# Optimization experiments

Hardware: AMD Instinct MI355X
Metric: run time of the kernel (lower is better)

The kernel has to match this reference:

```python
import jax, jax.numpy as jnp
import numpy as np
from functools import partial

# dims matching init_kwargs
H = 512      # hidden_size
F = 2048     # ff_size
NH = 8       # num_heads
NL = 6       # num_layers
V = 1024     # vocab_size
T = 8        # sentence_length
S = 5        # n_sentences_in_paragraph
P = 16       # n_paragraphs_in_article
L = P * S * T          # article_length = 640
N = L + 1              # sequence length used by masks = 641
B = 16                 # batch
HD = H // NH           # head dim
LN_EPS = 1e-5
NEG = -1e9


def _build_mask():
    # pseudo_causal_masks[0] from the torch __init__: causal ~tril plus
    # blocking of within-paragraph sentence-0 key columns.
    a = np.ones((P, S, T, P, S, T), dtype=bool)
    j = np.arange(P)
    a[j, :, :, j, 0, :] = False
    a = a.reshape(L, L)
    causal = ~np.tril(np.ones((N, N), dtype=bool))
    m = causal.copy()
    m[:-1, 1:] = np.logical_and(a, causal[:-1, 1:])
    return m  # True = disallowed


def _build_pe():
    # sinusoidal pe exactly as in __init__ (div_term uses hidden_size in denom)
    pos = np.arange(N, dtype=np.float32)[:, None]
    div = np.exp(np.arange(0, H // 2, dtype=np.float32) * (-np.log(10000.0) / H))
    pe = np.zeros((N, H), dtype=np.float32)
    pe[:, 0::2] = np.sin(pos * div)
    pe[:, 1::2] = np.cos(pos * div)
    return pe


def setup_inputs() -> dict:
    key = jax.random.key(0)
    ks = jax.random.split(key, 12)
    sd = 0.02
    inp = {
        'tokens': jax.random.randint(ks[0], (B, N), 0, V),
        'attn_mask': jnp.asarray(_build_mask()),
        'pe': jnp.asarray(_build_pe()),
        'emb': jax.random.normal(ks[1], (V, H), jnp.float32) * sd,
        'qkv_w': jax.random.normal(ks[2], (NL, 3 * H, H), jnp.float32) * sd,
        'qkv_b': jnp.zeros((NL, 3 * H), jnp.float32),
        'out_w': jax.random.normal(ks[3], (NL, H, H), jnp.float32) * sd,
        'out_b': jnp.zeros((NL, H), jnp.float32),
        'ln1_g': jnp.ones((NL, H), jnp.float32),
        'ln1_b': jnp.zeros((NL, H), jnp.float32),
        'fc1_w': jax.random.normal(ks[4], (NL, F, H), jnp.float32) * sd,
        'fc1_b': jnp.zeros((NL, F), jnp.float32),
        'fc2_w': jax.random.normal(ks[5], (NL, H, F), jnp.float32) * sd,
        'fc2_b': jnp.zeros((NL, H), jnp.float32),
        'ln2_g': jnp.ones((NL, H), jnp.float32),
        'ln2_b': jnp.zeros((NL, H), jnp.float32),
        'lnf_g': jnp.ones((H,), jnp.float32),
        'lnf_b': jnp.zeros((H,), jnp.float32),
        'dep_w': jax.random.normal(ks[6], (V, H), jnp.float32) * sd,
        'dep_b': jnp.zeros((V,), jnp.float32),
    }
    return inp


def _ln(x, g, b):
    m = jnp.mean(x, axis=-1, keepdims=True)
    v = jnp.mean(jnp.square(x - m), axis=-1, keepdims=True)
    return (x - m) * jax.lax.rsqrt(v + LN_EPS) * g + b


def _encoder_layer(x, p, mask):
    qw, qb, ow, ob, g1, b1, w1, bb1, w2, bb2, g2, b2 = p
    Bsz, Nn, _ = x.shape
    qkv = x @ qw.T + qb                                   # [B,N,3H]
    q, k, v = jnp.split(qkv, 3, axis=-1)
    q = q.reshape(Bsz, Nn, NH, HD)
    k = k.reshape(Bsz, Nn, NH, HD)
    v = v.reshape(Bsz, Nn, NH, HD)
    scores = jnp.einsum('bqhd,bkhd->bhqk', q, k) / jnp.sqrt(jnp.asarray(HD, x.dtype))
    scores = jnp.where(mask[None, None], NEG, scores)
    att = jax.nn.softmax(scores, axis=-1)
    o = jnp.einsum('bhqk,bkhd->bqhd', att, v).reshape(Bsz, Nn, H)
    o = o @ ow.T + ob
    x = _ln(x + o, g1, b1)                                # post-LN (torch default)
    f = jax.nn.gelu(x @ w1.T + bb1, approximate=False) @ w2.T + bb2
    return _ln(x + f, g2, b2)


def reference(tokens, attn_mask, pe, emb, qkv_w, qkv_b, out_w, out_b,
              ln1_g, ln1_b, fc1_w, fc1_b, fc2_w, fc2_b, ln2_g, ln2_b,
              lnf_g, lnf_b, dep_w, dep_b):
    x = emb[tokens] + pe[None]                            # [B,N,H]
    layers = (qkv_w, qkv_b, out_w, out_b, ln1_g, ln1_b,
              fc1_w, fc1_b, fc2_w, fc2_b, ln2_g, ln2_b)

    def step(h, p):
        return _encoder_layer(h, p, attn_mask), None

    x, _ = jax.lax.scan(step, x, layers)
    x = _ln(x, lnf_g, lnf_b)
    return x @ dep_w.T + dep_b                            # [B,N,V] logits
```

## Files before the change

kernel.cpp:

```cpp
#include <hip/hip_runtime.h>
#include <stdint.h>

#define NSEQ 641
#define BATCH 16
#define MROWS (BATCH * NSEQ)
#define HID 512
#define FFD 2048
#define NHEAD 8
#define HDIM 64
#define NLAYER 6
#define VOCAB 1024
#define KPAD 704

typedef __bf16 bf16x8 __attribute__((ext_vector_type(8)));
typedef float  f32x4  __attribute__((ext_vector_type(4)));
typedef int    i32x4  __attribute__((ext_vector_type(4)));
typedef short  s16x8  __attribute__((ext_vector_type(8)));
typedef short  s16x4  __attribute__((ext_vector_type(4)));

#define EXP_C 0.18033688011112042f

__device__ __forceinline__ uint32_t swz(uint32_t b) { return b ^ (((b >> 7) & 7u) << 4); }

__device__ __forceinline__ unsigned short f2bf(float f) {
  uint32_t u = __builtin_bit_cast(uint32_t, f);
  u += 0x7FFFu + ((u >> 16) & 1u);
  return (unsigned short)(u >> 16);
}

__device__ __forceinline__ void gload16(const void* g, void* l) {
  __builtin_amdgcn_global_load_lds(
      (const __attribute__((address_space(1))) uint32_t*)g,
      (__attribute__((address_space(3))) uint32_t*)l, 16, 0, 0);
}

__device__ __forceinline__ bf16x8 ld_lds16(const void* p) {
  return __builtin_bit_cast(bf16x8, *(const i32x4*)p);
}

__global__ void cvt_kernel(const float* __restrict__ in,
                           unsigned short* __restrict__ out, int n) {
  int i = (blockIdx.x * 256 + threadIdx.x) * 4;
  if (i >= n) return;
  f32x4 v = *(const f32x4*)(in + i);
  s16x4 o;
  o[0] = (short)f2bf(v[0]); o[1] = (short)f2bf(v[1]);
  o[2] = (short)f2bf(v[2]); o[3] = (short)f2bf(v[3]);
  *(s16x4*)(out + i) = o;
}

__global__ void embed_kernel(const int* __restrict__ tok,
                             const float* __restrict__ emb,
                             const float* __restrict__ pe,
                             float* __restrict__ x,
                             unsigned short* __restrict__ xb) {
  int m = blockIdx.x;
  int n = m % NSEQ;
  int t = tok[m];
  int h = threadIdx.x * 4;
  f32x4 e = *(const f32x4*)(emb + (size_t)t * HID + h);
  f32x4 p = *(const f32x4*)(pe + (size_t)n * HID + h);
  f32x4 v = e + p;
  *(f32x4*)(x + (size_t)m * HID + h) = v;
  s16x4 o;
  o[0] = (short)f2bf(v[0]); o[1] = (short)f2bf(v[1]);
  o[2] = (short)f2bf(v[2]); o[3] = (short)f2bf(v[3]);
  *(s16x4*)(xb + (size_t)m * HID + h) = o;
}

__global__ __launch_bounds__(256) void ln_kernel(
    const float* __restrict__ in, const float* __restrict__ gg,
    const float* __restrict__ bb, float* __restrict__ xo,
    unsigned short* __restrict__ xbo, int rows) {
  int row = blockIdx.x * 4 + (threadIdx.x >> 6);
  if (row >= rows) return;
  int lane = threadIdx.x & 63;
  const float* p = in + (size_t)row * HID + lane * 8;
  f32x4 a0 = *(const f32x4*)p;
  f32x4 a1 = *(const f32x4*)(p + 4);
  float s = a0[0] + a0[1] + a0[2] + a0[3] + a1[0] + a1[1] + a1[2] + a1[3];
#pragma unroll
  for (int o = 32; o; o >>= 1) s += __shfl_xor(s, o);
  float mean = s * (1.0f / HID);
  float vs = 0.f;
#pragma unroll
  for (int j = 0; j < 4; ++j) { float d = a0[j] - mean; vs += d * d; }
#pragma unroll
  for (int j = 0; j < 4; ++j) { float d = a1[j] - mean; vs += d * d; }
#pragma unroll
  for (int o = 32; o; o >>= 1) vs += __shfl_xor(vs, o);
  float rstd = rsqrtf(vs * (1.0f / HID) + 1e-5f);
  f32x4 g0 = *(const f32x4*)(gg + lane * 8);
  f32x4 g1 = *(const f32x4*)(gg + lane * 8 + 4);
  f32x4 b0 = *(const f32x4*)(bb + lane * 8);
  f32x4 b1 = *(const f32x4*)(bb + lane * 8 + 4);
  f32x4 y0, y1;
  s16x8 ob;
#pragma unroll
  for (int j = 0; j < 4; ++j) {
    y0[j] = (a0[j] - mean) * rstd * g0[j] + b0[j];
    y1[j] = (a1[j] - mean) * rstd * g1[j] + b1[j];
    ob[j] = (short)f2bf(y0[j]);
    ob[j + 4] = (short)f2bf(y1[j]);
  }
  float* xp = xo + (size_t)row * HID + lane * 8;
  *(f32x4*)xp = y0;
  *(f32x4*)(xp + 4) = y1;
  *(s16x8*)(xbo + (size_t)row * HID + lane * 8) = ob;
}

__global__ __launch_bounds__(256) void vtrans_kernel(
    const unsigned short* __restrict__ V, unsigned short* __restrict__ vT) {
  const int kt = blockIdx.x;
  const int bh = blockIdx.y;
  const int k0 = kt * 64;
  const int tid = threadIdx.x;
  __shared__ unsigned short lds[64][68];
  const size_t src = (size_t)bh * (NSEQ * HDIM);
#pragma unroll
  for (int it = 0; it < 2; ++it) {
    int k = it * 32 + (tid >> 3);
    int d0 = (tid & 7) * 8;
    int kr = k0 + k;
    s16x8 v = {};
    if (kr < NSEQ) v = *(const s16x8*)(V + src + (size_t)kr * HDIM + d0);
    *(s16x8*)&lds[k][d0] = v;
  }
  __syncthreads();
  const int d = tid & 63;
  const int w = tid >> 6;
  const size_t dst = ((size_t)bh * 64 + d) * KPAD + k0;
#pragma unroll
  for (int it = 0; it < 2; ++it) {
    int kc = w + it * 4;
    s16x8 o;
#pragma unroll
    for (int i = 0; i < 8; ++i) o[i] = lds[kc * 8 + i][d];
    *(s16x8*)(vT + dst + kc * 8) = o;
  }
}

enum { EPI_QKV = 0, EPI_GELU = 1, EPI_RESID = 2, EPI_F32OUT = 3 };

template <int EPI>
__global__ __launch_bounds__(256, 2) void gemm_bt(
    const unsigned short* __restrict__ A, const unsigned short* __restrict__ W,
    const float* __restrict__ bias, const float* __restrict__ resid,
    void* __restrict__ out0, void* __restrict__ out1, void* __restrict__ out2,
    int M, int N, int K) {
  __shared__ char sm[2][32768];
  const int tid = threadIdx.x, lane = tid & 63, wid = tid >> 6;
  const int wr = wid >> 1, wc = wid & 1;
  const int m0 = blockIdx.y * 128, n0 = blockIdx.x * 128;
  f32x4 acc[4][4] = {};
  const uint32_t Pbase = wid * 4096;

  auto stage = [&](int kt, char* dst) {
#pragma unroll
    for (int i = 0; i < 4; ++i) {
      uint32_t P = Pbase + i * 1024 + lane * 16;
      uint32_t L = swz(P);
      int row = (int)(L >> 7);
      uint32_t kb = L & 127u;
      int ma = m0 + row; if (ma >= M) ma = M - 1;
      gload16((const char*)A + ((size_t)ma * K + kt) * 2 + kb, dst + Pbase + i * 1024);
      gload16((const char*)W + ((size_t)(n0 + row) * K + kt) * 2 + kb,
              dst + 16384 + Pbase + i * 1024);
    }
  };

  const int nk = K >> 6;
  stage(0, sm[0]);
  __syncthreads();

  for (int t = 0; t < nk; ++t) {
    if (t + 1 < nk) stage((t + 1) << 6, sm[(t + 1) & 1]);
    const char* buf = sm[t & 1];
#pragma unroll
    for (int kk = 0; kk < 2; ++kk) {
      bf16x8 af[4], bfr[4];
#pragma unroll
      for (int mi = 0; mi < 4; ++mi) {
        int row = wr * 64 + mi * 16 + (lane & 15);
        af[mi] = ld_lds16(buf + swz((uint32_t)row * 128 + kk * 64 + ((lane >> 4) << 4)));
      }
#pragma unroll
      for (int ni = 0; ni < 4; ++ni) {
        int row = wc * 64 + ni * 16 + (lane & 15);
        bfr[ni] = ld_lds16(buf + 16384 + swz((uint32_t)row * 128 + kk * 64 + ((lane >> 4) << 4)));
      }
#pragma unroll
      for (int mi = 0; mi < 4; ++mi)
#pragma unroll
        for (int ni = 0; ni < 4; ++ni)
          acc[mi][ni] = __builtin_amdgcn_mfma_f32_16x16x32_bf16(af[mi], bfr[ni], acc[mi][ni], 0, 0, 0);
    }
    __syncthreads();
  }

#pragma unroll
  for (int mi = 0; mi < 4; ++mi) {
#pragma unroll
    for (int g = 0; g < 4; ++g) {
      int m = m0 + wr * 64 + mi * 16 + (lane >> 4) * 4 + g;
      if (m >= M) continue;
      int bbq = 0, nn = 0;
      if (EPI == EPI_QKV) { bbq = m / NSEQ; nn = m - bbq * NSEQ; }
#pragma unroll
      for (int ni = 0; ni < 4; ++ni) {
        int c = n0 + wc * 64 + ni * 16 + (lane & 15);
        float v = acc[mi][ni][g] + bias[c];
        if (EPI == EPI_QKV) {
          int which = c >> 9, hh = (c >> 6) & 7, d = c & 63;
          unsigned short* dst = which == 0 ? (unsigned short*)out0
                              : which == 1 ? (unsigned short*)out1
                                           : (unsigned short*)out2;
          dst[(((size_t)bbq * NHEAD + hh) * NSEQ + nn) * HDIM + d] = f2bf(v);
        } else if (EPI == EPI_GELU) {
          v = 0.5f * v * (1.0f + erff(v * 0.70710678118654752f));
          ((unsigned short*)out0)[(size_t)m * N + c] = f2bf(v);
        } else if (EPI == EPI_RESID) {
          float* o = (float*)out0;
          o[(size_t)m * N + c] = v + resid[(size_t)m * N + c];
        } else {
          ((float*)out0)[(size_t)m * N + c] = v;
        }
      }
    }
  }
}

__global__ __launch_bounds__(256) void attn_kernel(
    const unsigned short* __restrict__ Q, const unsigned short* __restrict__ Kb,
    const unsigned short* __restrict__ vT, unsigned short* __restrict__ O) {
  const int qt = blockIdx.x, bh = blockIdx.y;
  const int b = bh >> 3, h = bh & 7;
  const int q0 = qt * 64;
  const int tid = threadIdx.x, lane = tid & 63, w = tid >> 6;
  const int lg = lane >> 4, lc = lane & 15;
  __shared__ char sK[2][8192];
  __shared__ char sV[2][8192];
  __shared__ char sP[4][2048];

  const size_t base = (size_t)bh * (NSEQ * HDIM);
  const size_t baseT = (size_t)bh * (HDIM * KPAD);

  bf16x8 qf[2];
  {
    int qr = q0 + w * 16 + lc;
    if (qr > NSEQ - 1) qr = NSEQ - 1;
#pragma unroll
    for (int kk = 0; kk < 2; ++kk)
      qf[kk] = __builtin_bit_cast(
          bf16x8, *(const i32x4*)(Q + base + (size_t)qr * HDIM + kk * 32 + (lg << 3)));
  }

  f32x4 acc[4] = {};
  float lsum[4] = {0.f, 0.f, 0.f, 0.f};
  const int qrow_base = q0 + w * 16 + (lg << 2);

  int nkt = qt + 2;
  if (nkt > 11) nkt = 11;

  auto stage = [&](int kt, int bufi) {
    const int k0 = kt * 64;
#pragma unroll
    for (int i = 0; i < 2; ++i) {
      uint32_t P = w * 2048 + i * 1024 + lane * 16;
      uint32_t L = swz(P);
      int row = (int)(L >> 7);
      uint32_t kbyte = L & 127u;
      int kr = k0 + row; if (kr > NSEQ - 1) kr = NSEQ - 1;
      gload16((const char*)(Kb + base + (size_t)kr * HDIM) + kbyte,
              sK[bufi] + w * 2048 + i * 1024);
      gload16((const char*)(vT + baseT + (size_t)row * KPAD + k0) + kbyte,
              sV[bufi] + w * 2048 + i * 1024);
    }
  };

  stage(0, 0);
  __syncthreads();

  for (int kt = 0; kt < nkt; ++kt) {
    if (kt + 1 < nkt) stage(kt + 1, (kt + 1) & 1);
    const char* bK = sK[kt & 1];
    const char* bV = sV[kt & 1];
    const int k0 = kt * 64;

    f32x4 s[4] = {};
#pragma unroll
    for (int nt = 0; nt < 4; ++nt) {
#pragma unroll
      for (int kk = 0; kk < 2; ++kk) {
        int row = nt * 16 + lc;
        bf16x8 kf = ld_lds16(bK + swz((uint32_t)row * 128 + kk * 64 + (lg << 4)));
        s[nt] = __builtin_amdgcn_mfma_f32_16x16x32_bf16(qf[kk], kf, s[nt], 0, 0, 0);
      }
    }

    if (kt < qt) {
#pragma unroll
      for (int g = 0; g < 4; ++g)
#pragma unroll
        for (int nt = 0; nt < 4; ++nt) {
          float p = exp2f(s[nt][g] * EXP_C);
          s[nt][g] = p;
          lsum[g] += p;
        }
    } else if (kt == qt) {
#pragma unroll
      for (int g = 0; g < 4; ++g) {
        int q = qrow_base + g;
        int pp = q / 40;
        int lo = pp * 40 + 1, hi = pp * 40 + 8;
#pragma unroll
        for (int nt = 0; nt < 4; ++nt) {
          int k = k0 + nt * 16 + lc;
          bool ok = ((k <= q) || (k >= lo && k <= hi)) && (k < NSEQ);
          float p = ok ? exp2f(s[nt][g] * EXP_C) : 0.f;
          s[nt][g] = p;
          lsum[g] += p;
        }
      }
    } else {
#pragma unroll
      for (int g = 0; g < 4; ++g) {
        int q = qrow_base + g;
        int pp = q / 40;
        int lo = pp * 40 + 1, hi = pp * 40 + 8;
#pragma unroll
        for (int nt = 0; nt < 4; ++nt) {
          int k = k0 + nt * 16 + lc;
          bool ok = (k >= lo && k <= hi) && (k < NSEQ);
          float p = ok ? exp2f(s[nt][g] * EXP_C) : 0.f;
          s[nt][g] = p;
          lsum[g] += p;
        }
      }
    }

#pragma unroll
    for (int g = 0; g < 4; ++g) {
      int row = (lg << 2) + g;
#pragma unroll
      for (int nt = 0; nt < 4; ++nt) {
        int col = nt * 16 + lc;
        *(short*)(sP[w] + swz((uint32_t)row * 128 + col * 2)) = (short)f2bf(s[nt][g]);
      }
    }
#pragma unroll
    for (int kk = 0; kk < 2; ++kk) {
      bf16x8 pa = ld_lds16(sP[w] + swz((uint32_t)lc * 128 + kk * 64 + (lg << 4)));
#pragma unroll
      for (int nt = 0; nt < 4; ++nt) {
        int rowv = nt * 16 + lc;
        bf16x8 vf = ld_lds16(bV + swz((uint32_t)rowv * 128 + kk * 64 + (lg << 4)));
        acc[nt] = __builtin_amdgcn_mfma_f32_16x16x32_bf16(pa, vf, acc[nt], 0, 0, 0);
      }
    }
    __syncthreads();
  }

#pragma unroll
  for (int o = 1; o < 16; o <<= 1)
#pragma unroll
    for (int g = 0; g < 4; ++g) lsum[g] += __shfl_xor(lsum[g], o);

#pragma unroll
  for (int g = 0; g < 4; ++g) {
    int q = qrow_base + g;
    if (q >= NSEQ) continue;
    float inv = 1.0f / lsum[g];
#pragma unroll
    for (int nt = 0; nt < 4; ++nt) {
      int d = nt * 16 + lc;
      O[((size_t)b * NSEQ + q) * HID + h * HDIM + d] = f2bf(acc[nt][g] * inv);
    }
  }
}

extern "C" void kernel_launch(void* const* d_in, const int* in_sizes, int n_in,
                              void* d_out, int out_size, void* d_ws, size_t ws_size,
                              hipStream_t stream) {
  const int*   tok   = (const int*)d_in[0];
  const float* pe    = (const float*)d_in[2];
  const float* emb   = (const float*)d_in[3];
  const float* qkv_w = (const float*)d_in[4];
  const float* qkv_b = (const float*)d_in[5];
  const float* out_w = (const float*)d_in[6];
  const float* out_b = (const float*)d_in[7];
  const float* ln1_g = (const float*)d_in[8];
  const float* ln1_b = (const float*)d_in[9];
  const float* fc1_w = (const float*)d_in[10];
  const float* fc1_b = (const float*)d_in[11];
  const float* fc2_w = (const float*)d_in[12];
  const float* fc2_b = (const float*)d_in[13];
  const float* ln2_g = (const float*)d_in[14];
  const float* ln2_b = (const float*)d_in[15];
  const float* lnf_g = (const float*)d_in[16];
  const float* lnf_b = (const float*)d_in[17];
  const float* dep_w = (const float*)d_in[18];
  const float* dep_b = (const float*)d_in[19];

  const size_t SZ_QKV = (size_t)1536 * 512;
  const size_t SZ_OUT = (size_t)512 * 512;
  const size_t SZ_FC1 = (size_t)2048 * 512;
  const size_t SZ_FC2 = (size_t)512 * 2048;
  const size_t SZ_DEP = (size_t)VOCAB * 512;

  char* w = (char*)d_ws;
  float* x = (float*)w;            w += (size_t)MROWS * HID * 4;
  unsigned short* xb = (unsigned short*)w; w += (size_t)MROWS * HID * 2;
  unsigned short* qb = (unsigned short*)w; w += (size_t)BATCH * NHEAD * NSEQ * HDIM * 2;
  unsigned short* kb = (unsigned short*)w; w += (size_t)BATCH * NHEAD * NSEQ * HDIM * 2;
  unsigned short* vb = (unsigned short*)w; w += (size_t)BATCH * NHEAD * NSEQ * HDIM * 2;
  unsigned short* ao = (unsigned short*)w; w += (size_t)BATCH * NHEAD * NSEQ * HDIM * 2;
  unsigned short* mid = qb;
  unsigned short* vT = (unsigned short*)w; w += (size_t)BATCH * NHEAD * HDIM * KPAD * 2;

  size_t used = (size_t)(w - (char*)d_ws);
  size_t all_w_bytes = (NLAYER * (SZ_QKV + SZ_OUT + SZ_FC1 + SZ_FC2) + SZ_DEP) * 2;
  bool upfront = ws_size >= used + all_w_bytes;

  unsigned short *wq_all, *wo_all, *w1_all, *w2_all, *wd;
  if (upfront) {
    wq_all = (unsigned short*)w; w += NLAYER * SZ_QKV * 2;
    wo_all = (unsigned short*)w; w += NLAYER * SZ_OUT * 2;
    w1_all = (unsigned short*)w; w += NLAYER * SZ_FC1 * 2;
    w2_all = (unsigned short*)w; w += NLAYER * SZ_FC2 * 2;
    wd     = (unsigned short*)w; w += SZ_DEP * 2;
    cvt_kernel<<<dim3((NLAYER * SZ_QKV) / 1024), 256, 0, stream>>>(qkv_w, wq_all, NLAYER * SZ_QKV);
    cvt_kernel<<<dim3((NLAYER * SZ_OUT) / 1024), 256, 0, stream>>>(out_w, wo_all, NLAYER * SZ_OUT);
    cvt_kernel<<<dim3((NLAYER * SZ_FC1) / 1024), 256, 0, stream>>>(fc1_w, w1_all, NLAYER * SZ_FC1);
    cvt_kernel<<<dim3((NLAYER * SZ_FC2) / 1024), 256, 0, stream>>>(fc2_w, w2_all, NLAYER * SZ_FC2);
    cvt_kernel<<<dim3(SZ_DEP / 1024), 256, 0, stream>>>(dep_w, wd, SZ_DEP);
  } else {
    wq_all = (unsigned short*)w; w += SZ_QKV * 2;
    wo_all = (unsigned short*)w; w += SZ_OUT * 2;
    w1_all = (unsigned short*)w; w += SZ_FC1 * 2;
    w2_all = (unsigned short*)w; w += SZ_FC2 * 2;
    wd     = (unsigned short*)w; w += SZ_DEP * 2;
    cvt_kernel<<<dim3(SZ_DEP / 1024), 256, 0, stream>>>(dep_w, wd, SZ_DEP);
  }

  embed_kernel<<<dim3(MROWS), 128, 0, stream>>>(tok, emb, pe, x, xb);

  const int lnBlocks = (MROWS + 3) / 4;
  for (int l = 0; l < NLAYER; ++l) {
    unsigned short *wq, *wo, *w1, *w2;
    if (upfront) {
      wq = wq_all + l * SZ_QKV; wo = wo_all + l * SZ_OUT;
      w1 = w1_all + l * SZ_FC1; w2 = w2_all + l * SZ_FC2;
    } else {
      wq = wq_all; wo = wo_all; w1 = w1_all; w2 = w2_all;
      cvt_kernel<<<dim3(SZ_QKV / 1024), 256, 0, stream>>>(qkv_w + l * SZ_QKV, wq, SZ_QKV);
      cvt_kernel<<<dim3(SZ_OUT / 1024), 256, 0, stream>>>(out_w + l * SZ_OUT, wo, SZ_OUT);
      cvt_kernel<<<dim3(SZ_FC1 / 1024), 256, 0, stream>>>(fc1_w + l * SZ_FC1, w1, SZ_FC1);
      cvt_kernel<<<dim3(SZ_FC2 / 1024), 256, 0, stream>>>(fc2_w + l * SZ_FC2, w2, SZ_FC2);
    }

    gemm_bt<EPI_QKV><<<dim3(12, 81), 256, 0, stream>>>(
        xb, wq, qkv_b + l * 1536, nullptr, qb, kb, vb, MROWS, 1536, 512);
    vtrans_kernel<<<dim3(11, 128), 256, 0, stream>>>(vb, vT);
    attn_kernel<<<dim3(11, 128), 256, 0, stream>>>(qb, kb, vT, ao);
    gemm_bt<EPI_RESID><<<dim3(4, 81), 256, 0, stream>>>(
        ao, wo, out_b + l * 512, x, x, nullptr, nullptr, MROWS, 512, 512);
    ln_kernel<<<dim3(lnBlocks), 256, 0, stream>>>(x, ln1_g + l * 512, ln1_b + l * 512, x, xb, MROWS);
    gemm_bt<EPI_GELU><<<dim3(16, 81), 256, 0, stream>>>(
        xb, w1, fc1_b + l * 2048, nullptr, mid, nullptr, nullptr, MROWS, 2048, 512);
    gemm_bt<EPI_RESID><<<dim3(4, 81), 256, 0, stream>>>(
        mid, w2, fc2_b + l * 512, x, x, nullptr, nullptr, MROWS, 512, 2048);
    ln_kernel<<<dim3(lnBlocks), 256, 0, stream>>>(x, ln2_g + l * 512, ln2_b + l * 512, x, xb, MROWS);
  }

  ln_kernel<<<dim3(lnBlocks), 256, 0, stream>>>(x, lnf_g, lnf_b, x, xb, MROWS);
  gemm_bt<EPI_F32OUT><<<dim3(8, 81), 256, 0, stream>>>(
      xb, wd, dep_b, nullptr, d_out, nullptr, nullptr, MROWS, VOCAB, 512);
}
```

Baseline: 1.393 ms.

## Halve GEMM K-tile to raise occupancy and add XCD-aware block remapping

The GEMM K-step shrinks from 64 to 32, which halves shared memory per block and raises the launch-bounds target from 2 to 4 blocks per CU. It also switches to a new swizzle for the narrower tile. GEMM and attention grids become 1D, and a remap groups consecutive logical tiles onto the same XCD to improve L2 reuse. The trade-off is twice as many K iterations and barriers per tile, and possible register pressure under the tighter launch bound.

Measured after the change: 1.382 ms. No clear change (-0.8%).

```diff
diff --git a/kernel.cpp b/kernel.cpp
--- a/kernel.cpp
+++ b/kernel.cpp
@@ -21,6 +21,13 @@
 #define EXP_C 0.18033688011112042f
 
 __device__ __forceinline__ uint32_t swz(uint32_t b) { return b ^ (((b >> 7) & 7u) << 4); }
+__device__ __forceinline__ uint32_t swz32(uint32_t b) { return b ^ (((b >> 7) & 3u) << 4); }
+
+__device__ __forceinline__ int xcd_swz(int bid, int nwg) {
+  int x = bid & 7, j = bid >> 3;
+  int q = nwg >> 3, r = nwg & 7;
+  return x * q + (x < r ? x : r) + j;
+}
 
 __device__ __forceinline__ unsigned short f2bf(float f) {
   uint32_t u = __builtin_bit_cast(uint32_t, f);
@@ -143,58 +150,59 @@
 enum { EPI_QKV = 0, EPI_GELU = 1, EPI_RESID = 2, EPI_F32OUT = 3 };
 
 template <int EPI>
-__global__ __launch_bounds__(256, 2) void gemm_bt(
+__global__ __launch_bounds__(256, 4) void gemm_bt(
     const unsigned short* __restrict__ A, const unsigned short* __restrict__ W,
     const float* __restrict__ bias, const float* __restrict__ resid,
     void* __restrict__ out0, void* __restrict__ out1, void* __restrict__ out2,
     int M, int N, int K) {
-  __shared__ char sm[2][32768];
+  __shared__ char sm[2][16384];
   const int tid = threadIdx.x, lane = tid & 63, wid = tid >> 6;
   const int wr = wid >> 1, wc = wid & 1;
-  const int m0 = blockIdx.y * 128, n0 = blockIdx.x * 128;
+  const int lg = lane >> 4, lc = lane & 15;
+
+  const int nx = N >> 7;
+  const int logical = xcd_swz(blockIdx.x, gridDim.x);
+  const int m0 = (logical / nx) * 128, n0 = (logical % nx) * 128;
+
   f32x4 acc[4][4] = {};
-  const uint32_t Pbase = wid * 4096;
 
   auto stage = [&](int kt, char* dst) {
 #pragma unroll
-    for (int i = 0; i < 4; ++i) {
-      uint32_t P = Pbase + i * 1024 + lane * 16;
-      uint32_t L = swz(P);
-      int row = (int)(L >> 7);
-      uint32_t kb = L & 127u;
+    for (int i = 0; i < 2; ++i) {
+      uint32_t P = (uint32_t)tid * 16 + i * 4096;
+      uint32_t L = swz32(P);
+      int row = (int)(L >> 6);
+      uint32_t kb = L & 63u;
       int ma = m0 + row; if (ma >= M) ma = M - 1;
-      gload16((const char*)A + ((size_t)ma * K + kt) * 2 + kb, dst + Pbase + i * 1024);
+      gload16((const char*)A + ((size_t)ma * K + kt) * 2 + kb, dst + P);
       gload16((const char*)W + ((size_t)(n0 + row) * K + kt) * 2 + kb,
-              dst + 16384 + Pbase + i * 1024);
+              dst + 8192 + P);
     }
   };
 
-  const int nk = K >> 6;
+  const int nk = K >> 5;
   stage(0, sm[0]);
   __syncthreads();
 
   for (int t = 0; t < nk; ++t) {
-    if (t + 1 < nk) stage((t + 1) << 6, sm[(t + 1) & 1]);
+    if (t + 1 < nk) stage((t + 1) << 5, sm[(t + 1) & 1]);
     const char* buf = sm[t & 1];
-#pragma unroll
-    for (int kk = 0; kk < 2; ++kk) {
-      bf16x8 af[4], bfr[4];
-#pragma unroll
-      for (int mi = 0; mi < 4; ++mi) {
-        int row = wr * 64 + mi * 16 + (lane & 15);
-        af[mi] = ld_lds16(buf + swz((uint32_t)row * 128 + kk * 64 + ((lane >> 4) << 4)));
-      }
-#pragma unroll
-      for (int ni = 0; ni < 4; ++ni) {
-        int row = wc * 64 + ni * 16 + (lane & 15);
-        bfr[ni] = ld_lds16(buf + 16384 + swz((uint32_t)row * 128 + kk * 64 + ((lane >> 4) << 4)));
-      }
-#pragma unroll
-      for (int mi = 0; mi < 4; ++mi)
-#pragma unroll
-        for (int ni = 0; ni < 4; ++ni)
-          acc[mi][ni] = __builtin_amdgcn_mfma_f32_16x16x32_bf16(af[mi], bfr[ni], acc[mi][ni], 0, 0, 0);
-    }
+    bf16x8 af[4], bfr[4];
+#pragma unroll
+    for (int mi = 0; mi < 4; ++mi) {
+      int row = wr * 64 + mi * 16 + lc;
+      af[mi] = ld_lds16(buf + swz32((uint32_t)row * 64 + (lg << 4)));
+    }
+#pragma unroll
+    for (int ni = 0; ni < 4; ++ni) {
+      int row = wc * 64 + ni * 16 + lc;
+      bfr[ni] = ld_lds16(buf + 8192 + swz32((uint32_t)row * 64 + (lg << 4)));
+    }
+#pragma unroll
+    for (int mi = 0; mi < 4; ++mi)
+#pragma unroll
+      for (int ni = 0; ni < 4; ++ni)
+        acc[mi][ni] = __builtin_amdgcn_mfma_f32_16x16x32_bf16(af[mi], bfr[ni], acc[mi][ni], 0, 0, 0);
     __syncthreads();
   }
 
@@ -202,13 +210,13 @@
   for (int mi = 0; mi < 4; ++mi) {
 #pragma unroll
     for (int g = 0; g < 4; ++g) {
-      int m = m0 + wr * 64 + mi * 16 + (lane >> 4) * 4 + g;
+      int m = m0 + wr * 64 + mi * 16 + lg * 4 + g;
       if (m >= M) continue;
       int bbq = 0, nn = 0;
       if (EPI == EPI_QKV) { bbq = m / NSEQ; nn = m - bbq * NSEQ; }
 #pragma unroll
       for (int ni = 0; ni < 4; ++ni) {
-        int c = n0 + wc * 64 + ni * 16 + (lane & 15);
+        int c = n0 + wc * 64 + ni * 16 + lc;
         float v = acc[mi][ni][g] + bias[c];
         if (EPI == EPI_QKV) {
           int which = c >> 9, hh = (c >> 6) & 7, d = c & 63;
@@ -233,7 +241,8 @@
 __global__ __launch_bounds__(256) void attn_kernel(
     const unsigned short* __restrict__ Q, const unsigned short* __restrict__ Kb,
     const unsigned short* __restrict__ vT, unsigned short* __restrict__ O) {
-  const int qt = blockIdx.x, bh = blockIdx.y;
+  const int logical = xcd_swz(blockIdx.x, gridDim.x);
+  const int qt = logical % 11, bh = logical / 11;
   const int b = bh >> 3, h = bh & 7;
   const int q0 = qt * 64;
   const int tid = threadIdx.x, lane = tid & 63, w = tid >> 6;
@@ -459,21 +468,21 @@
       cvt_kernel<<<dim3(SZ_FC2 / 1024), 256, 0, stream>>>(fc2_w + l * SZ_FC2, w2, SZ_FC2);
     }
 
-    gemm_bt<EPI_QKV><<<dim3(12, 81), 256, 0, stream>>>(
+    gemm_bt<EPI_QKV><<<dim3(12 * 81), 256, 0, stream>>>(
         xb, wq, qkv_b + l * 1536, nullptr, qb, kb, vb, MROWS, 1536, 512);
     vtrans_kernel<<<dim3(11, 128), 256, 0, stream>>>(vb, vT);
-    attn_kernel<<<dim3(11, 128), 256, 0, stream>>>(qb, kb, vT, ao);
-    gemm_bt<EPI_RESID><<<dim3(4, 81), 256, 0, stream>>>(
+    attn_kernel<<<dim3(11 * 128), 256, 0, stream>>>(qb, kb, vT, ao);
+    gemm_bt<EPI_RESID><<<dim3(4 * 81), 256, 0, stream>>>(
         ao, wo, out_b + l * 512, x, x, nullptr, nullptr, MROWS, 512, 512);
     ln_kernel<<<dim3(lnBlocks), 256, 0, stream>>>(x, ln1_g + l * 512, ln1_b + l * 512, x, xb, MROWS);
-    gemm_bt<EPI_GELU><<<dim3(16, 81), 256, 0, stream>>>(
+    gemm_bt<EPI_GELU><<<dim3(16 * 81), 256, 0, stream>>>(
         xb, w1, fc1_b + l * 2048, nullptr, mid, nullptr, nullptr, MROWS, 2048, 512);
-    gemm_bt<EPI_RESID><<<dim3(4, 81), 256, 0, stream>>>(
+    gemm_bt<EPI_RESID><<<dim3(4 * 81), 256, 0, stream>>>(
         mid, w2, fc2_b + l * 512, x, x, nullptr, nullptr, MROWS, 512, 2048);
     ln_kernel<<<dim3(lnBlocks), 256, 0, stream>>>(x, ln2_g + l * 512, ln2_b + l * 512, x, xb, MROWS);
   }
 
   ln_kernel<<<dim3(lnBlocks), 256, 0, stream>>>(x, lnf_g, lnf_b, x, xb, MROWS);
-  gemm_bt<EPI_F32OUT><<<dim3(8, 81), 256, 0, stream>>>(
+  gemm_bt<EPI_F32OUT><<<dim3(8 * 81), 256, 0, stream>>>(
       xb, wd, dep_b, nullptr, d_out, nullptr, nullptr, MROWS, VOCAB, 512);
 }
```
